# Optimization experiments

Measured on AMD Instinct MI355X. Metric: run time of the kernel, lower is better.

The kernel has to match this reference:

```python
import jax, jax.numpy as jnp
import numpy as np

B, IN, HID, OUT, E, C, TOPK = 4096, 1024, 2048, 1024, 8, 1000, 2
EPS = 1e-6


def setup_inputs() -> dict:
    key = jax.random.key(0)
    ks = jax.random.split(key, 8)
    def xavier(k, fan_out, fan_in):
        lim = float(np.sqrt(6.0 / (fan_in + fan_out)))
        return jax.random.uniform(k, (fan_out, fan_in), jnp.float32, -lim, lim)
    return {
        "x": jax.random.normal(ks[0], (B, IN), jnp.float32),
        "Wg": xavier(ks[1], E, IN),
        "bg": jnp.zeros((E,), jnp.float32),
        "gamma": jnp.ones((1, E), jnp.float32),
        "beta": jnp.zeros((1, E), jnp.float32),
        "W1": xavier(ks[2], HID * E, IN),
        "b1": jnp.zeros((HID * E,), jnp.float32),
        "W2": xavier(ks[3], OUT * E, HID * E),
        "b2": jnp.zeros((OUT * E,), jnp.float32),
        "Wc": xavier(ks[4], C, OUT),
        "bc": jnp.zeros((C,), jnp.float32),
    }


def reference(x, Wg, bg, gamma, beta, W1, b1, W2, b2, Wc, bc):
    # gating (noise_std=0 -> no noise)
    gate_logits = x @ Wg.T + bg                      # [B, E]
    # GRN over expert dim
    Gx = jnp.linalg.norm(gate_logits, axis=1, keepdims=True)   # [B, 1]
    Nx = Gx / (jnp.mean(Gx, axis=0, keepdims=True) + EPS)      # [B, 1]
    gate_logits = gamma * (gate_logits * Nx) + beta
    gate_probs = jax.nn.softmax(gate_logits, axis=-1)
    topk_probs, topk_idx = jax.lax.top_k(gate_probs, TOPK)     # [B, K]
    # dense all-expert MLP (fc2 mixes across ALL experts' hidden units, as in source)
    h = jax.nn.relu(x @ W1.T + b1)                   # [B, HID*E]
    eo = (h @ W2.T + b2).reshape(B, E, OUT)          # [B, E, OUT]
    sel = jnp.take_along_axis(eo, topk_idx[:, :, None], axis=1)  # [B, K, OUT]
    out = jnp.einsum('bk,bkd->bd', topk_probs, sel)  # [B, OUT]
    return out @ Wc.T + bc                           # [B, C]
```

## Files before the change

### kernel.cpp

```cpp
#include <hip/hip_runtime.h>
#include <stdint.h>

#define B_SZ   4096
#define IN_SZ  1024
#define NE     8
#define NC     1000
#define HIDE   16384
#define OUTE   1024
#define GEPS   1e-6f
#define NSPLIT 2
#define KSPL   8192

#define W2TOT  134217728
#define SA     33554432
#define SB     41943040
#define SC     25165824
#define SD     12582912
#define SE     20971520

typedef __attribute__((ext_vector_type(8))) short short8;
typedef __attribute__((ext_vector_type(4))) float floatx4;

__device__ __forceinline__ unsigned short f2bf(float f) {
    unsigned u = __float_as_uint(f);
    u += 0x7fffu + ((u >> 16) & 1u);
    return (unsigned short)(u >> 16);
}
__device__ __forceinline__ float bf2f(unsigned short h) {
    return __uint_as_float(((unsigned)h) << 16);
}

__device__ __forceinline__ void async16(const void* g, void* l) {
    __builtin_amdgcn_global_load_lds(
        (const __attribute__((address_space(1))) void*)g,
        (__attribute__((address_space(3))) void*)l, 16, 0, 0);
}

__device__ __forceinline__ void cvt_span(const float* __restrict__ src,
                                         unsigned short* __restrict__ dst,
                                         int n, int bid, int nb) {
    const int bdim = (int)blockDim.x;
    int i = (bid * bdim + (int)threadIdx.x) * 8;
    int stride = nb * bdim * 8;
    for (; i < n; i += stride) {
        float4 v0 = *(const float4*)(src + i);
        float4 v1 = *(const float4*)(src + i + 4);
        uint4 w;
        w.x = (unsigned)f2bf(v0.x) | ((unsigned)f2bf(v0.y) << 16);
        w.y = (unsigned)f2bf(v0.z) | ((unsigned)f2bf(v0.w) << 16);
        w.z = (unsigned)f2bf(v1.x) | ((unsigned)f2bf(v1.y) << 16);
        w.w = (unsigned)f2bf(v1.z) | ((unsigned)f2bf(v1.w) << 16);
        *(uint4*)(dst + i) = w;
    }
}

__global__ __launch_bounds__(256) void k_gatef(const float* __restrict__ x,
                                               const float* __restrict__ Wg,
                                               const float* __restrict__ bg,
                                               float* __restrict__ logits,
                                               float* __restrict__ Gx,
                                               unsigned short* __restrict__ xb,
                                               const float* __restrict__ W1,
                                               unsigned short* __restrict__ w1b,
                                               const float* __restrict__ Wc,
                                               unsigned short* __restrict__ wcb,
                                               const float* __restrict__ W2,
                                               unsigned short* __restrict__ w2b) {
    const int bid = blockIdx.x;
    if (bid >= 1024) {
        if (bid < 1536)      cvt_span(W1, w1b, HIDE * IN_SZ, bid - 1024, 512);
        else if (bid < 1600) cvt_span(Wc, wcb, NC * IN_SZ,   bid - 1536, 64);
        else                 cvt_span(W2, w2b, SA,           bid - 1600, 1024);
        return;
    }
    int wid = threadIdx.x >> 6, lane = threadIdx.x & 63;
    int b = bid * 4 + wid;
    const float* xr = x + (size_t)b * IN_SZ;
    float xv[16];
#pragma unroll
    for (int t = 0; t < 16; ++t) xv[t] = xr[lane + 64 * t];
    unsigned short* xbr = xb + (size_t)b * IN_SZ;
#pragma unroll
    for (int t = 0; t < 16; ++t) xbr[lane + 64 * t] = f2bf(xv[t]);
    float lg[NE];
#pragma unroll
    for (int e = 0; e < NE; ++e) {
        const float* wr = Wg + e * IN_SZ;
        float s = 0.f;
#pragma unroll
        for (int t = 0; t < 16; ++t) s += xv[t] * wr[lane + 64 * t];
#pragma unroll
        for (int m = 32; m >= 1; m >>= 1) s += __shfl_xor(s, m, 64);
        lg[e] = s + bg[e];
    }
    if (lane == 0) {
        float ss = 0.f;
#pragma unroll
        for (int e = 0; e < NE; ++e) { logits[b * NE + e] = lg[e]; ss += lg[e] * lg[e]; }
        Gx[b] = sqrtf(ss);
    }
}

__global__ __launch_bounds__(1024) void k_gsumf(const float* __restrict__ Gx,
                                                float* __restrict__ gsum, int* __restrict__ ctrl,
                                                const float* __restrict__ W2,
                                                unsigned short* __restrict__ w2b) {
    if (blockIdx.x > 0) {
        cvt_span(W2 + SA, w2b + SA, SB, blockIdx.x - 1, 2047);
        return;
    }
    __shared__ float sm[1024];
    int t = threadIdx.x;
    if (t < 24) ctrl[t] = 0;
    sm[t] = Gx[t] + Gx[t + 1024] + Gx[t + 2048] + Gx[t + 3072];
    __syncthreads();
    for (int m = 512; m >= 1; m >>= 1) {
        if (t < m) sm[t] += sm[t + m];
        __syncthreads();
    }
    if (t == 0) gsum[0] = sm[0];
}

__global__ __launch_bounds__(256) void k_topkf(const float* __restrict__ logits,
                                               const float* __restrict__ Gx,
                                               const float* __restrict__ gsum,
                                               const float* __restrict__ gamma,
                                               const float* __restrict__ beta,
                                               int* __restrict__ tidx, float* __restrict__ tp,
                                               int* __restrict__ counts,
                                               const float* __restrict__ W2,
                                               unsigned short* __restrict__ w2b) {
    if (blockIdx.x >= 16) {
        cvt_span(W2 + (SA + SB), w2b + (SA + SB), SC, blockIdx.x - 16, 1024);
        return;
    }
    int b = blockIdx.x * 256 + threadIdx.x;
    float nx = Gx[b] / (gsum[0] * (1.0f / (float)B_SZ) + GEPS);
    float l[NE];
    float mx = -1e30f;
#pragma unroll
    for (int e = 0; e < NE; ++e) {
        l[e] = gamma[e] * (logits[b * NE + e] * nx) + beta[e];
        mx = fmaxf(mx, l[e]);
    }
    float se = 0.f;
#pragma unroll
    for (int e = 0; e < NE; ++e) { l[e] = expf(l[e] - mx); se += l[e]; }
    float inv = 1.f / se;
    int i0 = 0; float p0 = l[0];
#pragma unroll
    for (int e = 1; e < NE; ++e) if (l[e] > p0) { p0 = l[e]; i0 = e; }
    int i1 = -1; float p1 = -1.f;
#pragma unroll
    for (int e = 0; e < NE; ++e) if (e != i0 && l[e] > p1) { p1 = l[e]; i1 = e; }
    tidx[b * 2 + 0] = i0; tidx[b * 2 + 1] = i1;
    tp[b * 2 + 0] = p0 * inv; tp[b * 2 + 1] = p1 * inv;
    atomicAdd(&counts[i0], 1);
    atomicAdd(&counts[i1], 1);
}

__global__ __launch_bounds__(256) void k_offsetsf(const int* __restrict__ counts,
                                                  int* __restrict__ offs,
                                                  const float* __restrict__ W2,
                                                  unsigned short* __restrict__ w2b) {
    if (blockIdx.x > 0) {
        cvt_span(W2 + (SA + SB + SC), w2b + (SA + SB + SC), SD, blockIdx.x - 1, 511);
        return;
    }
    if (threadIdx.x == 0) {
        int a = 0;
        for (int e = 0; e < NE; ++e) { offs[e] = a; a += counts[e]; }
    }
}

__global__ __launch_bounds__(256) void k_fillf(const int* __restrict__ tidx, const float* __restrict__ tp,
                                               const int* __restrict__ offs, int* __restrict__ cursors,
                                               int* __restrict__ rowsw, int* __restrict__ slotof,
                                               const float* __restrict__ W2,
                                               unsigned short* __restrict__ w2b) {
    if (blockIdx.x >= 16) {
        cvt_span(W2 + (SA + SB + SC + SD), w2b + (SA + SB + SC + SD), SE, blockIdx.x - 16, 1008);
        return;
    }
    int b = blockIdx.x * 256 + threadIdx.x;
#pragma unroll
    for (int k = 0; k < 2; ++k) {
        int e = tidx[b * 2 + k];
        int pos = atomicAdd(&cursors[e], 1);
        int at = offs[e] + pos;
        rowsw[at] = b * 2 + k;
        slotof[b * 2 + k] = at;
    }
}


__device__ __forceinline__ void compute_bk64(const short* buf, const int* aoff, const int* boff,
                                             floatx4 acc[4][4]) {
    const short* sA = buf;
    const short* sB = buf + 8192;
    short8 a0[4], a1[4], b0[4], b1[4];
#pragma unroll
    for (int i = 0; i < 4; ++i) {
        a0[i] = *(const short8*)(sA + aoff[i]);
        a1[i] = *(const short8*)(sA + (aoff[i] ^ 32));
        b0[i] = *(const short8*)(sB + boff[i]);
        b1[i] = *(const short8*)(sB + (boff[i] ^ 32));
    }
    asm volatile("s_waitcnt lgkmcnt(0)" ::: "memory");
    __builtin_amdgcn_sched_barrier(0);
    __builtin_amdgcn_s_setprio(1);
#pragma unroll
    for (int i = 0; i < 4; ++i)
#pragma unroll
        for (int j = 0; j < 4; ++j) {
            acc[i][j] = __builtin_amdgcn_mfma_f32_16x16x32_bf16(a0[i], b0[j], acc[i][j], 0, 0, 0);
            acc[i][j] = __builtin_amdgcn_mfma_f32_16x16x32_bf16(a1[i], b1[j], acc[i][j], 0, 0, 0);
        }
    __builtin_amdgcn_s_setprio(0);
}

__device__ __forceinline__ void stage_bk64(const unsigned short* const* pa,
                                           const unsigned short* const* pb,
                                           char* bufc, int koff, int tid) {
#pragma unroll
    for (int c = 0; c < 4; ++c) {
        async16(pa[c] + koff, bufc + c * 4096 + tid * 16);
        async16(pb[c] + koff, bufc + 16384 + c * 4096 + tid * 16);
    }
}

__device__ __forceinline__ void core64db(const unsigned short* const* pa,
                                         const unsigned short* const* pb,
                                         short* smem, int nkt, int wm, int wn,
                                         int tid, int lane, floatx4 acc[4][4]) {
    char* b0c = (char*)smem;
    char* b1c = b0c + 32768;
    const int sl = ((lane >> 4) ^ (lane & 7)) * 8;
    int aoff[4], boff[4];
#pragma unroll
    for (int i = 0; i < 4; ++i) {
        aoff[i] = (wm * 64 + i * 16 + (lane & 15)) * 64 + sl;
        boff[i] = (wn * 64 + i * 16 + (lane & 15)) * 64 + sl;
    }
    stage_bk64(pa, pb, b0c, 0, tid);
    __syncthreads();
#pragma unroll 1
    for (int kt = 0; kt < nkt; kt += 2) {
        if (kt + 1 < nkt) stage_bk64(pa, pb, b1c, (kt + 1) * 64, tid);
        compute_bk64(smem, aoff, boff, acc);
        __syncthreads();
        if (kt + 2 < nkt) stage_bk64(pa, pb, b0c, (kt + 2) * 64, tid);
        compute_bk64(smem + 16384, aoff, boff, acc);
        __syncthreads();
    }
}

__global__ __launch_bounds__(256) void k_h8(const unsigned short* __restrict__ xb,
                                            const unsigned short* __restrict__ w1b,
                                            const float* __restrict__ b1,
                                            unsigned short* __restrict__ hout) {
    extern __shared__ short smem[];
    const int tid = threadIdx.x, lane = tid & 63, wid = tid >> 6;
    const int wm = wid >> 1, wn = wid & 1;
    const int wg = (blockIdx.x & 7) * (gridDim.x >> 3) + (blockIdx.x >> 3);
    const int mt = wg & 31, nt = wg >> 5;
    const int m0 = mt * 128, n0 = nt * 128;
    const int srow = tid >> 3;
    const int cswz = ((tid & 7) ^ (srow & 7)) * 8;
    const unsigned short* pa[4];
    const unsigned short* pb[4];
#pragma unroll
    for (int c = 0; c < 4; ++c) {
        pa[c] = xb  + (size_t)(m0 + 32 * c + srow) * IN_SZ + cswz;
        pb[c] = w1b + (size_t)(n0 + 32 * c + srow) * IN_SZ + cswz;
    }
    floatx4 acc[4][4] = {};
    core64db(pa, pb, smem, IN_SZ / 64, wm, wn, tid, lane, acc);
#pragma unroll
    for (int i = 0; i < 4; ++i)
#pragma unroll
        for (int j = 0; j < 4; ++j)
#pragma unroll
            for (int r = 0; r < 4; ++r) {
                int row = m0 + wm * 64 + i * 16 + (lane >> 4) * 4 + r;
                int col = n0 + wn * 64 + j * 16 + (lane & 15);
                float v = acc[i][j][r] + b1[col];
                hout[(size_t)row * HIDE + col] = f2bf(fmaxf(v, 0.f));
            }
}

__global__ __launch_bounds__(256) void k_moe(const unsigned short* __restrict__ h,
                                             const unsigned short* __restrict__ w2b,
                                             const int* __restrict__ counts,
                                             const int* __restrict__ offs,
                                             const int* __restrict__ rowsw,
                                             unsigned short* __restrict__ parts) {
    const int wg = (blockIdx.x & 7) * (gridDim.x >> 3) + (blockIdx.x >> 3);
    const int mt = wg & 31, nt = (wg >> 5) & 7, sp = (wg >> 8) & 1, e = wg >> 9;
    const int gn = counts[e];
    if (mt * 128 >= gn) return;
    const int gbase = offs[e];
    extern __shared__ short smem[];
    const int tid = threadIdx.x, lane = tid & 63, wid = tid >> 6;
    const int wm = wid >> 1, wn = wid & 1;
    const int srow = tid >> 3;
    const int cswz = ((tid & 7) ^ (srow & 7)) * 8;
    const unsigned short* pa[4];
    const unsigned short* pb[4];
#pragma unroll
    for (int c = 0; c < 4; ++c) {
        int lr = mt * 128 + 32 * c + srow;
        if (lr > gn - 1) lr = gn - 1;
        int grow = rowsw[gbase + lr] >> 1;
        pa[c] = h + (size_t)grow * HIDE + sp * KSPL + cswz;
        pb[c] = w2b + (size_t)(e * OUTE + nt * 128 + 32 * c + srow) * HIDE + sp * KSPL + cswz;
    }
    floatx4 acc[4][4] = {};
    core64db(pa, pb, smem, KSPL / 64, wm, wn, tid, lane, acc);
    unsigned short* pbase = parts + (size_t)sp * B_SZ * 2 * OUTE;
#pragma unroll
    for (int i = 0; i < 4; ++i)
#pragma unroll
        for (int j = 0; j < 4; ++j)
#pragma unroll
            for (int r = 0; r < 4; ++r) {
                int lr = mt * 128 + wm * 64 + i * 16 + (lane >> 4) * 4 + r;
                if (lr < gn) {
                    int at = gbase + lr;
                    int col = nt * 128 + wn * 64 + j * 16 + (lane & 15);
                    pbase[(size_t)at * OUTE + col] = f2bf(acc[i][j][r]);
                }
            }
}

__global__ __launch_bounds__(256) void k_reduce(const unsigned short* __restrict__ parts,
                                                const int* __restrict__ slotof,
                                                const int* __restrict__ tidx,
                                                const float* __restrict__ tp,
                                                const float* __restrict__ b2,
                                                unsigned short* __restrict__ ymix) {
    int i = blockIdx.x * 256 + threadIdx.x;
    int b = i >> 8, col = (i & 255) * 4;
    int at0 = slotof[b * 2], at1 = slotof[b * 2 + 1];
    int e0 = tidx[b * 2], e1 = tidx[b * 2 + 1];
    float q0 = tp[b * 2], q1 = tp[b * 2 + 1];
    float y0[4] = {0.f, 0.f, 0.f, 0.f}, y1[4] = {0.f, 0.f, 0.f, 0.f};
#pragma unroll
    for (int sp = 0; sp < NSPLIT; ++sp) {
        ushort4 u0 = *(const ushort4*)(parts + ((size_t)sp * B_SZ * 2 + at0) * OUTE + col);
        ushort4 u1 = *(const ushort4*)(parts + ((size_t)sp * B_SZ * 2 + at1) * OUTE + col);
        y0[0] += bf2f(u0.x); y0[1] += bf2f(u0.y); y0[2] += bf2f(u0.z); y0[3] += bf2f(u0.w);
        y1[0] += bf2f(u1.x); y1[1] += bf2f(u1.y); y1[2] += bf2f(u1.z); y1[3] += bf2f(u1.w);
    }
    float4 bb0 = *(const float4*)(b2 + (size_t)e0 * OUTE + col);
    float4 bb1 = *(const float4*)(b2 + (size_t)e1 * OUTE + col);
    ushort4 o;
    o.x = f2bf(q0 * (y0[0] + bb0.x) + q1 * (y1[0] + bb1.x));
    o.y = f2bf(q0 * (y0[1] + bb0.y) + q1 * (y1[1] + bb1.y));
    o.z = f2bf(q0 * (y0[2] + bb0.z) + q1 * (y1[2] + bb1.z));
    o.w = f2bf(q0 * (y0[3] + bb0.w) + q1 * (y1[3] + bb1.w));
    *(ushort4*)(ymix + (size_t)b * OUTE + col) = o;
}

__global__ __launch_bounds__(256) void k_gemm_out(const unsigned short* __restrict__ ymix,
                                                  const unsigned short* __restrict__ wcb,
                                                  const float* __restrict__ bc,
                                                  float* __restrict__ out) {
    const int mt = blockIdx.x >> 3, nt = blockIdx.x & 7;
    const int m0 = mt * 128, n0 = nt * 128;
    extern __shared__ short smem[];
    const int tid = threadIdx.x, lane = tid & 63, wid = tid >> 6;
    const int wm = wid >> 1, wn = wid & 1;
    const int srow = tid >> 3;
    const int cswz = ((tid & 7) ^ (srow & 7)) * 8;
    const unsigned short* pa[4];
    const unsigned short* pb[4];
#pragma unroll
    for (int c = 0; c < 4; ++c) {
        pa[c] = ymix + (size_t)(m0 + 32 * c + srow) * IN_SZ + cswz;
        int br = n0 + 32 * c + srow; if (br > NC - 1) br = NC - 1;
        pb[c] = wcb + (size_t)br * IN_SZ + cswz;
    }
    floatx4 acc[4][4] = {};
    core64db(pa, pb, smem, IN_SZ / 64, wm, wn, tid, lane, acc);
#pragma unroll
    for (int i = 0; i < 4; ++i)
#pragma unroll
        for (int j = 0; j < 4; ++j)
#pragma unroll
            for (int r = 0; r < 4; ++r) {
                int row = m0 + wm * 64 + i * 16 + (lane >> 4) * 4 + r;
                int col = n0 + wn * 64 + j * 16 + (lane & 15);
                if (col < NC)
                    out[(size_t)row * NC + col] = acc[i][j][r] + bc[col];
            }
}

extern "C" void kernel_launch(void* const* d_in, const int* in_sizes, int n_in,
                              void* d_out, int out_size, void* d_ws, size_t ws_size,
                              hipStream_t stream) {
    const float* x     = (const float*)d_in[0];
    const float* Wg    = (const float*)d_in[1];
    const float* bg    = (const float*)d_in[2];
    const float* gamma = (const float*)d_in[3];
    const float* beta  = (const float*)d_in[4];
    const float* W1    = (const float*)d_in[5];
    const float* b1    = (const float*)d_in[6];
    const float* W2    = (const float*)d_in[7];
    const float* b2    = (const float*)d_in[8];
    const float* Wc    = (const float*)d_in[9];
    const float* bc    = (const float*)d_in[10];
    float* out = (float*)d_out;

    char* ws = (char*)d_ws;
    size_t o = 0;
    auto carve = [&](size_t bytes) { char* p = ws + o; o += (bytes + 255) & ~(size_t)255; return p; };
    unsigned short* xb    = (unsigned short*)carve((size_t)B_SZ * IN_SZ * 2);
    unsigned short* w1b   = (unsigned short*)carve((size_t)HIDE * IN_SZ * 2);
    unsigned short* w2b   = (unsigned short*)carve((size_t)NE * OUTE * HIDE * 2);
    unsigned short* wcb   = (unsigned short*)carve((size_t)NC * IN_SZ * 2);
    unsigned short* h     = (unsigned short*)carve((size_t)B_SZ * HIDE * 2);
    unsigned short* parts = (unsigned short*)carve((size_t)NSPLIT * B_SZ * 2 * OUTE * 2);
    unsigned short* ymix  = (unsigned short*)carve((size_t)B_SZ * OUTE * 2);
    float* logits = (float*)carve((size_t)B_SZ * NE * 4);
    float* Gx     = (float*)carve((size_t)B_SZ * 4);
    int*   tidx   = (int*)carve((size_t)B_SZ * 2 * 4);
    float* tp     = (float*)carve((size_t)B_SZ * 2 * 4);
    int*   rowsw  = (int*)carve((size_t)B_SZ * 2 * 4);
    int*   slotof = (int*)carve((size_t)B_SZ * 2 * 4);
    int*   ctrl   = (int*)carve(256);
    int* counts  = ctrl;
    int* cursors = ctrl + 8;
    int* offs    = ctrl + 16;
    float* gsum  = (float*)(ctrl + 24);

    hipFuncSetAttribute((const void*)k_h8,       hipFuncAttributeMaxDynamicSharedMemorySize, 65536);
    hipFuncSetAttribute((const void*)k_moe,      hipFuncAttributeMaxDynamicSharedMemorySize, 65536);
    hipFuncSetAttribute((const void*)k_gemm_out, hipFuncAttributeMaxDynamicSharedMemorySize, 65536);

    k_gatef<<<2624, 256, 0, stream>>>(x, Wg, bg, logits, Gx, xb, W1, w1b, Wc, wcb, W2, w2b);
    k_gsumf<<<2048, 1024, 0, stream>>>(Gx, gsum, ctrl, W2, w2b);
    k_topkf<<<1040, 256, 0, stream>>>(logits, Gx, gsum, gamma, beta, tidx, tp, counts, W2, w2b);
    k_offsetsf<<<512, 256, 0, stream>>>(counts, offs, W2, w2b);
    k_fillf<<<1024, 256, 0, stream>>>(tidx, tp, offs, cursors, rowsw, slotof, W2, w2b);

    k_h8<<<(B_SZ / 128) * (HIDE / 128), 256, 65536, stream>>>(xb, w1b, b1, h);
    k_moe<<<NE * 32 * 8 * NSPLIT, 256, 65536, stream>>>(h, w2b, counts, offs, rowsw, parts);
    k_reduce<<<B_SZ, 256, 0, stream>>>(parts, slotof, tidx, tp, b2, ymix);
    k_gemm_out<<<(B_SZ / 128) * 8, 256, 65536, stream>>>(ymix, wcb, bc, out);
}
```

Before: 881.5 us.

## Use 256x128 tiles with BK=32 for the hidden and expert GEMMs

Changes the k_h8 and k_moe GEMM tiles from 128x128 with BK=64 to 256x128 with BK=32. Each wave now holds an 8x4 accumulator block, which raises arithmetic intensity per LDS load and halves the number of global reads of the weight operand. Shared memory drops to 48KB, with a new swizzle for 32-wide rows. The trade-offs are higher register pressure, which may lower occupancy, more k-iterations with barriers, and more wasted rows in partially filled expert tiles. k_gemm_out keeps the old BK64 path, moved lower in the file.

```diff
diff --git a/kernel.cpp b/kernel.cpp
--- a/kernel.cpp
+++ b/kernel.cpp
@@ -11,7 +11,6 @@
 #define NSPLIT 2
 #define KSPL   8192
 
-#define W2TOT  134217728
 #define SA     33554432
 #define SB     41943040
 #define SC     25165824
@@ -194,63 +193,60 @@
 }
 
 
-__device__ __forceinline__ void compute_bk64(const short* buf, const int* aoff, const int* boff,
-                                             floatx4 acc[4][4]) {
+__device__ __forceinline__ void stage32(const unsigned short* const* pa,
+                                        const unsigned short* const* pb,
+                                        char* bufc, int koff, int tid) {
+#pragma unroll
+    for (int c = 0; c < 4; ++c)
+        async16(pa[c] + koff, bufc + c * 4096 + tid * 16);
+#pragma unroll
+    for (int c = 0; c < 2; ++c)
+        async16(pb[c] + koff, bufc + 16384 + c * 4096 + tid * 16);
+}
+
+__device__ __forceinline__ void compute32(const short* buf, const int* aoff, const int* boff,
+                                          floatx4 acc[8][4]) {
     const short* sA = buf;
     const short* sB = buf + 8192;
-    short8 a0[4], a1[4], b0[4], b1[4];
-#pragma unroll
-    for (int i = 0; i < 4; ++i) {
-        a0[i] = *(const short8*)(sA + aoff[i]);
-        a1[i] = *(const short8*)(sA + (aoff[i] ^ 32));
-        b0[i] = *(const short8*)(sB + boff[i]);
-        b1[i] = *(const short8*)(sB + (boff[i] ^ 32));
-    }
+    short8 av[8], bv[4];
+#pragma unroll
+    for (int i = 0; i < 8; ++i) av[i] = *(const short8*)(sA + aoff[i]);
+#pragma unroll
+    for (int j = 0; j < 4; ++j) bv[j] = *(const short8*)(sB + boff[j]);
     asm volatile("s_waitcnt lgkmcnt(0)" ::: "memory");
     __builtin_amdgcn_sched_barrier(0);
     __builtin_amdgcn_s_setprio(1);
 #pragma unroll
-    for (int i = 0; i < 4; ++i)
-#pragma unroll
-        for (int j = 0; j < 4; ++j) {
-            acc[i][j] = __builtin_amdgcn_mfma_f32_16x16x32_bf16(a0[i], b0[j], acc[i][j], 0, 0, 0);
-            acc[i][j] = __builtin_amdgcn_mfma_f32_16x16x32_bf16(a1[i], b1[j], acc[i][j], 0, 0, 0);
-        }
+    for (int i = 0; i < 8; ++i)
+#pragma unroll
+        for (int j = 0; j < 4; ++j)
+            acc[i][j] = __builtin_amdgcn_mfma_f32_16x16x32_bf16(av[i], bv[j], acc[i][j], 0, 0, 0);
     __builtin_amdgcn_s_setprio(0);
 }
 
-__device__ __forceinline__ void stage_bk64(const unsigned short* const* pa,
-                                           const unsigned short* const* pb,
-                                           char* bufc, int koff, int tid) {
-#pragma unroll
-    for (int c = 0; c < 4; ++c) {
-        async16(pa[c] + koff, bufc + c * 4096 + tid * 16);
-        async16(pb[c] + koff, bufc + 16384 + c * 4096 + tid * 16);
-    }
-}
-
-__device__ __forceinline__ void core64db(const unsigned short* const* pa,
+__device__ __forceinline__ void core32db(const unsigned short* const* pa,
                                          const unsigned short* const* pb,
                                          short* smem, int nkt, int wm, int wn,
-                                         int tid, int lane, floatx4 acc[4][4]) {
+                                         int tid, int lane, floatx4 acc[8][4]) {
     char* b0c = (char*)smem;
-    char* b1c = b0c + 32768;
-    const int sl = ((lane >> 4) ^ (lane & 7)) * 8;
-    int aoff[4], boff[4];
-#pragma unroll
-    for (int i = 0; i < 4; ++i) {
-        aoff[i] = (wm * 64 + i * 16 + (lane & 15)) * 64 + sl;
-        boff[i] = (wn * 64 + i * 16 + (lane & 15)) * 64 + sl;
-    }
-    stage_bk64(pa, pb, b0c, 0, tid);
+    char* b1c = b0c + 24576;
+    const int soff = ((lane >> 4) ^ ((lane >> 1) & 3)) * 8;
+    int aoff[8], boff[4];
+#pragma unroll
+    for (int i = 0; i < 8; ++i)
+        aoff[i] = (wm * 128 + i * 16 + (lane & 15)) * 32 + soff;
+#pragma unroll
+    for (int j = 0; j < 4; ++j)
+        boff[j] = (wn * 64 + j * 16 + (lane & 15)) * 32 + soff;
+    stage32(pa, pb, b0c, 0, tid);
     __syncthreads();
 #pragma unroll 1
     for (int kt = 0; kt < nkt; kt += 2) {
-        if (kt + 1 < nkt) stage_bk64(pa, pb, b1c, (kt + 1) * 64, tid);
-        compute_bk64(smem, aoff, boff, acc);
+        if (kt + 1 < nkt) stage32(pa, pb, b1c, (kt + 1) * 32, tid);
+        compute32(smem, aoff, boff, acc);
         __syncthreads();
-        if (kt + 2 < nkt) stage_bk64(pa, pb, b0c, (kt + 2) * 64, tid);
-        compute_bk64(smem + 16384, aoff, boff, acc);
+        if (kt + 2 < nkt) stage32(pa, pb, b0c, (kt + 2) * 32, tid);
+        compute32(smem + 12288, aoff, boff, acc);
         __syncthreads();
     }
 }
@@ -263,26 +259,27 @@
     const int tid = threadIdx.x, lane = tid & 63, wid = tid >> 6;
     const int wm = wid >> 1, wn = wid & 1;
     const int wg = (blockIdx.x & 7) * (gridDim.x >> 3) + (blockIdx.x >> 3);
-    const int mt = wg & 31, nt = wg >> 5;
-    const int m0 = mt * 128, n0 = nt * 128;
-    const int srow = tid >> 3;
-    const int cswz = ((tid & 7) ^ (srow & 7)) * 8;
+    const int mt = wg & 15, nt = wg >> 4;
+    const int m0 = mt * 256, n0 = nt * 128;
+    const int sr = tid >> 2;
+    const int chk = (tid & 3) ^ ((tid >> 3) & 3);
     const unsigned short* pa[4];
-    const unsigned short* pb[4];
-#pragma unroll
-    for (int c = 0; c < 4; ++c) {
-        pa[c] = xb  + (size_t)(m0 + 32 * c + srow) * IN_SZ + cswz;
-        pb[c] = w1b + (size_t)(n0 + 32 * c + srow) * IN_SZ + cswz;
-    }
-    floatx4 acc[4][4] = {};
-    core64db(pa, pb, smem, IN_SZ / 64, wm, wn, tid, lane, acc);
-#pragma unroll
-    for (int i = 0; i < 4; ++i)
+    const unsigned short* pb[2];
+#pragma unroll
+    for (int c = 0; c < 4; ++c)
+        pa[c] = xb + (size_t)(m0 + 64 * c + sr) * IN_SZ + chk * 8;
+#pragma unroll
+    for (int c = 0; c < 2; ++c)
+        pb[c] = w1b + (size_t)(n0 + 64 * c + sr) * IN_SZ + chk * 8;
+    floatx4 acc[8][4] = {};
+    core32db(pa, pb, smem, IN_SZ / 32, wm, wn, tid, lane, acc);
+#pragma unroll
+    for (int i = 0; i < 8; ++i)
 #pragma unroll
         for (int j = 0; j < 4; ++j)
 #pragma unroll
             for (int r = 0; r < 4; ++r) {
-                int row = m0 + wm * 64 + i * 16 + (lane >> 4) * 4 + r;
+                int row = m0 + wm * 128 + i * 16 + (lane >> 4) * 4 + r;
                 int col = n0 + wn * 64 + j * 16 + (lane & 15);
                 float v = acc[i][j][r] + b1[col];
                 hout[(size_t)row * HIDE + col] = f2bf(fmaxf(v, 0.f));
@@ -296,35 +293,37 @@
                                              const int* __restrict__ rowsw,
                                              unsigned short* __restrict__ parts) {
     const int wg = (blockIdx.x & 7) * (gridDim.x >> 3) + (blockIdx.x >> 3);
-    const int mt = wg & 31, nt = (wg >> 5) & 7, sp = (wg >> 8) & 1, e = wg >> 9;
+    const int mt = wg & 15, nt = (wg >> 4) & 7, sp = (wg >> 7) & 1, e = wg >> 8;
     const int gn = counts[e];
-    if (mt * 128 >= gn) return;
+    if (mt * 256 >= gn) return;
     const int gbase = offs[e];
     extern __shared__ short smem[];
     const int tid = threadIdx.x, lane = tid & 63, wid = tid >> 6;
     const int wm = wid >> 1, wn = wid & 1;
-    const int srow = tid >> 3;
-    const int cswz = ((tid & 7) ^ (srow & 7)) * 8;
+    const int sr = tid >> 2;
+    const int chk = (tid & 3) ^ ((tid >> 3) & 3);
     const unsigned short* pa[4];
-    const unsigned short* pb[4];
+    const unsigned short* pb[2];
 #pragma unroll
     for (int c = 0; c < 4; ++c) {
-        int lr = mt * 128 + 32 * c + srow;
+        int lr = mt * 256 + 64 * c + sr;
         if (lr > gn - 1) lr = gn - 1;
         int grow = rowsw[gbase + lr] >> 1;
-        pa[c] = h + (size_t)grow * HIDE + sp * KSPL + cswz;
-        pb[c] = w2b + (size_t)(e * OUTE + nt * 128 + 32 * c + srow) * HIDE + sp * KSPL + cswz;
-    }
-    floatx4 acc[4][4] = {};
-    core64db(pa, pb, smem, KSPL / 64, wm, wn, tid, lane, acc);
+        pa[c] = h + (size_t)grow * HIDE + sp * KSPL + chk * 8;
+    }
+#pragma unroll
+    for (int c = 0; c < 2; ++c)
+        pb[c] = w2b + (size_t)(e * OUTE + nt * 128 + 64 * c + sr) * HIDE + sp * KSPL + chk * 8;
+    floatx4 acc[8][4] = {};
+    core32db(pa, pb, smem, KSPL / 32, wm, wn, tid, lane, acc);
     unsigned short* pbase = parts + (size_t)sp * B_SZ * 2 * OUTE;
 #pragma unroll
-    for (int i = 0; i < 4; ++i)
+    for (int i = 0; i < 8; ++i)
 #pragma unroll
         for (int j = 0; j < 4; ++j)
 #pragma unroll
             for (int r = 0; r < 4; ++r) {
-                int lr = mt * 128 + wm * 64 + i * 16 + (lane >> 4) * 4 + r;
+                int lr = mt * 256 + wm * 128 + i * 16 + (lane >> 4) * 4 + r;
                 if (lr < gn) {
                     int at = gbase + lr;
                     int col = nt * 128 + wn * 64 + j * 16 + (lane & 15);
@@ -360,6 +359,67 @@
     o.z = f2bf(q0 * (y0[2] + bb0.z) + q1 * (y1[2] + bb1.z));
     o.w = f2bf(q0 * (y0[3] + bb0.w) + q1 * (y1[3] + bb1.w));
     *(ushort4*)(ymix + (size_t)b * OUTE + col) = o;
+}
+
+__device__ __forceinline__ void compute_bk64(const short* buf, const int* aoff, const int* boff,
+                                             floatx4 acc[4][4]) {
+    const short* sA = buf;
+    const short* sB = buf + 8192;
+    short8 a0[4], a1[4], b0[4], b1[4];
+#pragma unroll
+    for (int i = 0; i < 4; ++i) {
+        a0[i] = *(const short8*)(sA + aoff[i]);
+        a1[i] = *(const short8*)(sA + (aoff[i] ^ 32));
+        b0[i] = *(const short8*)(sB + boff[i]);
+        b1[i] = *(const short8*)(sB + (boff[i] ^ 32));
+    }
+    asm volatile("s_waitcnt lgkmcnt(0)" ::: "memory");
+    __builtin_amdgcn_sched_barrier(0);
+    __builtin_amdgcn_s_setprio(1);
+#pragma unroll
+    for (int i = 0; i < 4; ++i)
+#pragma unroll
+        for (int j = 0; j < 4; ++j) {
+            acc[i][j] = __builtin_amdgcn_mfma_f32_16x16x32_bf16(a0[i], b0[j], acc[i][j], 0, 0, 0);
+            acc[i][j] = __builtin_amdgcn_mfma_f32_16x16x32_bf16(a1[i], b1[j], acc[i][j], 0, 0, 0);
+        }
+    __builtin_amdgcn_s_setprio(0);
+}
+
+__device__ __forceinline__ void stage_bk64(const unsigned short* const* pa,
+                                           const unsigned short* const* pb,
+                                           char* bufc, int koff, int tid) {
+#pragma unroll
+    for (int c = 0; c < 4; ++c) {
+        async16(pa[c] + koff, bufc + c * 4096 + tid * 16);
+        async16(pb[c] + koff, bufc + 16384 + c * 4096 + tid * 16);
+    }
+}
+
+__device__ __forceinline__ void core64db(const unsigned short* const* pa,
+                                         const unsigned short* const* pb,
+                                         short* smem, int nkt, int wm, int wn,
+                                         int tid, int lane, floatx4 acc[4][4]) {
+    char* b0c = (char*)smem;
+    char* b1c = b0c + 32768;
+    const int sl = ((lane >> 4) ^ (lane & 7)) * 8;
+    int aoff[4], boff[4];
+#pragma unroll
+    for (int i = 0; i < 4; ++i) {
+        aoff[i] = (wm * 64 + i * 16 + (lane & 15)) * 64 + sl;
+        boff[i] = (wn * 64 + i * 16 + (lane & 15)) * 64 + sl;
+    }
+    stage_bk64(pa, pb, b0c, 0, tid);
+    __syncthreads();
+#pragma unroll 1
+    for (int kt = 0; kt < nkt; kt += 2) {
+        if (kt + 1 < nkt) stage_bk64(pa, pb, b1c, (kt + 1) * 64, tid);
+        compute_bk64(smem, aoff, boff, acc);
+        __syncthreads();
+        if (kt + 2 < nkt) stage_bk64(pa, pb, b0c, (kt + 2) * 64, tid);
+        compute_bk64(smem + 16384, aoff, boff, acc);
+        __syncthreads();
+    }
 }
 
 __global__ __launch_bounds__(256) void k_gemm_out(const unsigned short* __restrict__ ymix,
@@ -434,8 +494,8 @@
     int* offs    = ctrl + 16;
     float* gsum  = (float*)(ctrl + 24);
 
-    hipFuncSetAttribute((const void*)k_h8,       hipFuncAttributeMaxDynamicSharedMemorySize, 65536);
-    hipFuncSetAttribute((const void*)k_moe,      hipFuncAttributeMaxDynamicSharedMemorySize, 65536);
+    hipFuncSetAttribute((const void*)k_h8,       hipFuncAttributeMaxDynamicSharedMemorySize, 49152);
+    hipFuncSetAttribute((const void*)k_moe,      hipFuncAttributeMaxDynamicSharedMemorySize, 49152);
     hipFuncSetAttribute((const void*)k_gemm_out, hipFuncAttributeMaxDynamicSharedMemorySize, 65536);
 
     k_gatef<<<2624, 256, 0, stream>>>(x, Wg, bg, logits, Gx, xb, W1, w1b, Wc, wcb, W2, w2b);
@@ -444,8 +504,8 @@
     k_offsetsf<<<512, 256, 0, stream>>>(counts, offs, W2, w2b);
     k_fillf<<<1024, 256, 0, stream>>>(tidx, tp, offs, cursors, rowsw, slotof, W2, w2b);
 
-    k_h8<<<(B_SZ / 128) * (HIDE / 128), 256, 65536, stream>>>(xb, w1b, b1, h);
-    k_moe<<<NE * 32 * 8 * NSPLIT, 256, 65536, stream>>>(h, w2b, counts, offs, rowsw, parts);
+    k_h8<<<(B_SZ / 256) * (HIDE / 128), 256, 49152, stream>>>(xb, w1b, b1, h);
+    k_moe<<<NE * NSPLIT * 8 * 16, 256, 49152, stream>>>(h, w2b, counts, offs, rowsw, parts);
     k_reduce<<<B_SZ, 256, 0, stream>>>(parts, slotof, tidx, tp, b2, ymix);
     k_gemm_out<<<(B_SZ / 128) * 8, 256, 65536, stream>>>(ymix, wcb, bc, out);
 }
```

Result: slower. 1.457 ms (+65.3%).
